# Kernel tuning notes

Hardware: AMD Instinct MI355X
Metric: run time of the kernel (lower is better)

The kernel has to match this reference:

```python
import jax, jax.numpy as jnp
import numpy as np

N_EMBD = 384
NUM_HEADS = 6


def setup_inputs() -> dict:
    key = jax.random.key(0)
    k1, k2, k3 = jax.random.split(key, 3)
    b, t = 128, 256
    X = jax.random.normal(k1, (b, t, N_EMBD), dtype=jnp.float32)
    Wqkv = jax.random.normal(k2, (N_EMBD, 3 * N_EMBD), dtype=jnp.float32) * 0.02
    Wproj = jax.random.normal(k3, (N_EMBD, N_EMBD), dtype=jnp.float32) * 0.02
    return {"X": X, "Wqkv": Wqkv, "Wproj": Wproj}


def reference(X, Wqkv, Wproj):
    b, t, c = X.shape
    d = c // NUM_HEADS
    # fused QKV projection; split order in the source is K, Q, V
    qkv = X @ Wqkv  # (b, t, 3c)
    K, Q, V = jnp.split(qkv, 3, axis=-1)
    # (b, t, H, d) -> (b, H, t, d)
    K = K.reshape(b, t, NUM_HEADS, d).transpose(0, 2, 1, 3)
    Q = Q.reshape(b, t, NUM_HEADS, d).transpose(0, 2, 1, 3)
    V = V.reshape(b, t, NUM_HEADS, d).transpose(0, 2, 1, 3)
    # NOTE: faithful quirk — scale by full embed dim c, not head_size
    scale = c ** (-0.5)
    W = jnp.einsum("bhqd,bhkd->bhqk", Q, K) * scale  # (b, H, t, t)
    causal = jnp.tril(jnp.ones((t, t), dtype=bool))
    W = jnp.where(causal, W, -jnp.inf)
    W = jax.nn.softmax(W, axis=-1)
    # dropout layers are identity in eval mode
    OUT = jnp.einsum("bhqk,bhkd->bhqd", W, V)  # (b, H, t, d)
    OUT = OUT.transpose(0, 2, 1, 3).reshape(b, t, c)
    return OUT @ Wproj
```

## Files before the change

### kernel.cpp

```cpp
#include <hip/hip_runtime.h>
#include <hip/hip_bf16.h>

#define BATCH 128
#define TSEQ  256
#define NEMBD 384
#define NHEAD 6
#define HDIM  64
#define C3    1152
#define MROWS 32768
#define KGTOT 48
#define NBH   768
#define BHSZ  16384

#define NA_CH  (MROWS * KGTOT)
#define NW1_CH (C3 * KGTOT)
#define NW2_CH (NEMBD * KGTOT)

#define XBLOCKS 2048
#define WBLOCKS 288

typedef __attribute__((ext_vector_type(8))) short short8v;
typedef __attribute__((ext_vector_type(4))) float float4v;


__device__ __forceinline__ float bf2f(unsigned short u) {
  union { unsigned int i; float f; } x;
  x.i = ((unsigned int)u) << 16;
  return x.f;
}

__device__ __forceinline__ unsigned short f2bf(float f) {
  __hip_bfloat16 h = __float2bfloat16(f);
  unsigned short u;
  __builtin_memcpy(&u, &h, 2);
  return u;
}

__device__ __forceinline__ void convB_body(const float* __restrict__ W,
                                           unsigned short* __restrict__ out,
                                           int N, int idx) {
  const int nl  = idx & 127;
  const int kgg = (idx >> 7) % KGTOT;
  const int nb  = idx / (128 * KGTOT);
  const int n = nb * 128 + nl;
  short8v v;
#pragma unroll
  for (int j = 0; j < 8; ++j)
    v[j] = (short)f2bf(W[(size_t)(kgg * 8 + j) * N + n]);
  *reinterpret_cast<short8v*>(out + (size_t)idx * 8) = v;
}

__global__ __launch_bounds__(256)
void convert_all(const float* __restrict__ X, const float* __restrict__ W1,
                 const float* __restrict__ W2, unsigned short* __restrict__ Abf,
                 unsigned short* __restrict__ W1T, unsigned short* __restrict__ W2T) {
  const int tid = threadIdx.x;
  if (blockIdx.x < XBLOCKS) {
    __shared__ __attribute__((aligned(16))) unsigned short T[16][392];
    const int rb = blockIdx.x;
    const float* Xb = X + (size_t)rb * 16 * NEMBD;
#pragma unroll
    for (int i = 0; i < 6; ++i) {
      const int f4 = i * 256 + tid;
      const float4 v = reinterpret_cast<const float4*>(Xb)[f4];
      const int r = f4 / 96;
      const int c = (f4 % 96) * 4;
      ushort4 u;
      u.x = f2bf(v.x); u.y = f2bf(v.y); u.z = f2bf(v.z); u.w = f2bf(v.w);
      *reinterpret_cast<ushort4*>(&T[r][c]) = u;
    }
    __syncthreads();
#pragma unroll
    for (int i = 0; i < 3; ++i) {
      const int c2   = i * 256 + tid;
      const int kgg  = c2 >> 4;
      const int ml16 = c2 & 15;
      const short8v v = *reinterpret_cast<const short8v*>(&T[ml16][kgg * 8]);
      const int m  = rb * 16 + ml16;
      const int mb = m >> 7;
      const int ml = m & 127;
      *reinterpret_cast<short8v*>(Abf + ((size_t)(mb * KGTOT + kgg) * 128 + ml) * 8) = v;
    }
  } else {
    const int wi = (blockIdx.x - XBLOCKS) * 256 + tid;
    if (wi < NW1_CH) convB_body(W1, W1T, C3, wi);
    else             convB_body(W2, W2T, NEMBD, wi - NW1_CH);
  }
}


#define GEMM_STAGE(Ab, Bb, kb, ASL, BSL)                                               \
  _Pragma("unroll") for (int r = 0; r < 2; ++r) {                                      \
    const int i = r * 256 + tid;                                                       \
    const size_t goff = ((size_t)((kb) * 4 + (i >> 7)) * 128 + (i & 127)) * 8;         \
    __builtin_amdgcn_global_load_lds(                                                  \
        (const __attribute__((address_space(1))) unsigned int*)((Ab) + goff),          \
        (__attribute__((address_space(3))) unsigned int*)((ASL) + i * 8), 16, 0, 0);   \
    __builtin_amdgcn_global_load_lds(                                                  \
        (const __attribute__((address_space(1))) unsigned int*)((Bb) + goff),          \
        (__attribute__((address_space(3))) unsigned int*)((BSL) + i * 8), 16, 0, 0);   \
  }

#define GEMM_CORE(Ab, Bb)                                                              \
  __shared__ __attribute__((aligned(16))) unsigned short S[16384];                     \
  const int tid  = threadIdx.x;                                                        \
  const int wave = tid >> 6;                                                           \
  const int lane = tid & 63;                                                           \
  const int wm  = (wave & 1) * 64;                                                     \
  const int wn  = (wave >> 1) * 64;                                                    \
  const int l15 = lane & 15;                                                           \
  const int lq  = lane >> 4;                                                           \
  float4v acc[4][4];                                                                   \
  _Pragma("unroll") for (int i = 0; i < 4; ++i)                                        \
    _Pragma("unroll") for (int j = 0; j < 4; ++j)                                      \
      acc[i][j] = (float4v){0.f, 0.f, 0.f, 0.f};                                       \
  GEMM_STAGE(Ab, Bb, 0, S, S + 4096)                                                   \
  for (int kb = 0; kb < KGTOT / 4; ++kb) {                                             \
    const int cur = (kb & 1) * 8192;                                                   \
    const int nxt = 8192 - cur;                                                        \
    __syncthreads();                                                                   \
    if (kb + 1 < KGTOT / 4) {                                                          \
      GEMM_STAGE(Ab, Bb, kb + 1, S + nxt, S + nxt + 4096)                              \
    }                                                                                  \
    short8v af[4], bfr[4];                                                             \
    _Pragma("unroll") for (int mi = 0; mi < 4; ++mi)                                   \
      af[mi] = *reinterpret_cast<const short8v*>(                                      \
          S + cur + (size_t)(lq * 128 + wm + mi * 16 + l15) * 8);                      \
    _Pragma("unroll") for (int ni = 0; ni < 4; ++ni)                                   \
      bfr[ni] = *reinterpret_cast<const short8v*>(                                     \
          S + cur + 4096 + (size_t)(lq * 128 + wn + ni * 16 + l15) * 8);               \
    _Pragma("unroll") for (int mi = 0; mi < 4; ++mi)                                   \
      _Pragma("unroll") for (int ni = 0; ni < 4; ++ni)                                 \
        acc[mi][ni] = __builtin_amdgcn_mfma_f32_16x16x32_bf16(af[mi], bfr[ni],         \
                                                              acc[mi][ni], 0, 0, 0);   \
  }

__global__ __launch_bounds__(256)
void gemm_qkv(const unsigned short* __restrict__ A,
              const unsigned short* __restrict__ B,
              unsigned short* __restrict__ KQV) {
  const int ord   = blockIdx.x;
  const int xcd   = ord & 7;
  const int g     = ord >> 3;
  const int mtile = xcd * 32 + (g & 31);
  const int ntile = g >> 5;
  const unsigned short* Ab = A + (size_t)mtile * (KGTOT * 128 * 8);
  const unsigned short* Bb = B + (size_t)ntile * (KGTOT * 128 * 8);
  GEMM_CORE(Ab, Bb)
  const int colb = ntile * 128 + wn + l15;
  const int rowb = mtile * 128 + wm + lq * 4;
  if (ntile >= 6) {
    unsigned short* Vb = KQV + (size_t)(2 * NBH) * BHSZ;
#pragma unroll
    for (int ni = 0; ni < 4; ++ni) {
      const int rem = colb + ni * 16 - 768;
      const int hh  = rem >> 6;
      const int d   = rem & 63;
#pragma unroll
      for (int mi = 0; mi < 4; ++mi) {
        const int m  = rowb + mi * 16;
        const int bb = m >> 8;
        const int tt = m & 255;
        ushort4 v;
        v.x = f2bf(acc[mi][ni][0]); v.y = f2bf(acc[mi][ni][1]);
        v.z = f2bf(acc[mi][ni][2]); v.w = f2bf(acc[mi][ni][3]);
        *reinterpret_cast<ushort4*>(
            Vb + (size_t)(bb * NHEAD + hh) * BHSZ + (tt >> 3) * 512 + d * 8 + (tt & 7)) = v;
      }
    }
  } else {
    const int type = (ntile >= 3) ? 1 : 0;
    const float sc = type ? 0.051031036307982884f : 1.0f;
    unsigned short* outb = KQV + (size_t)type * NBH * BHSZ;
    const int hp = ntile - type * 3;
    const int bb = mtile >> 1;
    const int t0 = (mtile & 1) * 128;
    __syncthreads();
#pragma unroll
    for (int ni = 0; ni < 4; ++ni) {
      const int lc = wn + ni * 16 + l15;
      const int c8 = lc >> 3;
      const int dl = lc & 7;
#pragma unroll
      for (int mi = 0; mi < 4; ++mi) {
        const int lr0 = wm + lq * 4 + mi * 16;
#pragma unroll
        for (int r = 0; r < 4; ++r)
          S[(size_t)(c8 * 128 + lr0 + r) * 8 + dl] = f2bf(acc[mi][ni][r] * sc);
      }
    }
    __syncthreads();
#pragma unroll
    for (int it = 0; it < 8; ++it) {
      const int f  = it * 2048 + tid * 8;
      const int c8 = f >> 10;
      const int lr = (f >> 3) & 127;
      const int hh = hp * 2 + (c8 >> 3);
      const int dg = c8 & 7;
      *reinterpret_cast<short8v*>(
          outb + (size_t)(bb * NHEAD + hh) * BHSZ + dg * 2048 + (size_t)(t0 + lr) * 8) =
          *reinterpret_cast<const short8v*>(S + f);
    }
  }
}

__global__ __launch_bounds__(256)
void gemm_proj(const unsigned short* __restrict__ A,
               const unsigned short* __restrict__ B,
               float* __restrict__ C, int N) {
  const int ord   = blockIdx.x;
  const int xcd   = ord & 7;
  const int g     = ord >> 3;
  const int mtile = xcd * 32 + (g & 31);
  const int ntile = g >> 5;
  const unsigned short* Ab = A + (size_t)mtile * (KGTOT * 128 * 8);
  const unsigned short* Bb = B + (size_t)ntile * (KGTOT * 128 * 8);
  GEMM_CORE(Ab, Bb)
  float* Sf = reinterpret_cast<float*>(S);
#pragma unroll
  for (int pass = 0; pass < 2; ++pass) {
    __syncthreads();
    if ((wave & 1) == pass) {
#pragma unroll
      for (int mi = 0; mi < 4; ++mi)
#pragma unroll
        for (int ni = 0; ni < 4; ++ni)
#pragma unroll
          for (int r = 0; r < 4; ++r)
            Sf[(lq * 4 + mi * 16 + r) * 128 + (wn + ni * 16 + l15)] = acc[mi][ni][r];
    }
    __syncthreads();
    const int rowstart = mtile * 128 + pass * 64;
#pragma unroll
    for (int it = 0; it < 8; ++it) {
      const int f  = it * 1024 + tid * 4;
      const int lr = f >> 7;
      const int lc = f & 127;
      *reinterpret_cast<float4*>(&C[(size_t)(rowstart + lr) * N + ntile * 128 + lc]) =
          *reinterpret_cast<const float4*>(&Sf[f]);
    }
  }
}

__global__ __launch_bounds__(256, 3)
void attn_mfma(const unsigned short* __restrict__ KQV,
               unsigned short* __restrict__ Obf) {
  const int bh   = blockIdx.x;
  const int b    = bh / NHEAD;
  const int h    = bh - b * NHEAD;
  const int tid  = threadIdx.x;
  const int wave = tid >> 6;
  const int lane = tid & 63;
  const int l15  = lane & 15;
  const int lq   = lane >> 4;

  __shared__ __attribute__((aligned(16))) unsigned short Kls[16384];
  __shared__ __attribute__((aligned(16))) unsigned short Pt[4][1024];

  const unsigned short* Kb = KQV + (size_t)bh * BHSZ;
  const unsigned short* Qb = KQV + (size_t)(NBH + bh) * BHSZ;
  const unsigned short* Vb = KQV + (size_t)(2 * NBH + bh) * BHSZ;

#pragma unroll
  for (int r = 0; r < 8; ++r) {
    const int i = r * 256 + tid;
    __builtin_amdgcn_global_load_lds(
        (const __attribute__((address_space(1))) unsigned int*)(Kb + (size_t)i * 8),
        (__attribute__((address_space(3))) unsigned int*)(Kls + i * 8), 16, 0, 0);
  }
  __syncthreads();

  unsigned short* Pw = Pt[wave];

  for (int j = 0; j < 4; ++j) {
    short8v qa[2];
#pragma unroll
    for (int s = 0; s < 2; ++s)
      qa[s] = *reinterpret_cast<const short8v*>(
          Qb + (size_t)(s * 4 + lq) * 2048 + (size_t)(j * 64 + wave * 16 + l15) * 8);

    float4v o[4];
#pragma unroll
    for (int nf = 0; nf < 4; ++nf) o[nf] = (float4v){0.f, 0.f, 0.f, 0.f};
    float4v lp = (float4v){0.f, 0.f, 0.f, 0.f};

    for (int kt = 0; kt <= j; ++kt) {
      short8v vf[2][4];
#pragma unroll
      for (int s = 0; s < 2; ++s)
#pragma unroll
        for (int nf = 0; nf < 4; ++nf)
          vf[s][nf] = *reinterpret_cast<const short8v*>(
              Vb + (size_t)(kt * 8 + s * 4 + lq) * 512 + (size_t)(nf * 16 + l15) * 8);

      float4v sf[4];
#pragma unroll
      for (int nf = 0; nf < 4; ++nf) sf[nf] = (float4v){0.f, 0.f, 0.f, 0.f};
#pragma unroll
      for (int s = 0; s < 2; ++s) {
        short8v kf[4];
#pragma unroll
        for (int nf = 0; nf < 4; ++nf)
          kf[nf] = *reinterpret_cast<const short8v*>(
              Kls + (size_t)(s * 4 + lq) * 2048 + (size_t)(kt * 64 + nf * 16 + l15) * 8);
#pragma unroll
        for (int nf = 0; nf < 4; ++nf)
          sf[nf] = __builtin_amdgcn_mfma_f32_16x16x32_bf16(qa[s], kf[nf], sf[nf], 0, 0, 0);
      }

      if (kt == j) {
        const int qit = wave * 16 + lq * 4;
#pragma unroll
        for (int nf = 0; nf < 4; ++nf) {
          const int key = nf * 16 + l15;
#pragma unroll
          for (int r = 0; r < 4; ++r)
            if (key > qit + r) sf[nf][r] = -INFINITY;
        }
      }

#pragma unroll
      for (int nf = 0; nf < 4; ++nf) {
        const int kg  = nf * 2 + (l15 >> 3);
        const int pos = l15 & 7;
#pragma unroll
        for (int r = 0; r < 4; ++r) {
          const float p = __expf(sf[nf][r]);
          lp[r] += p;
          Pw[(kg * 16 + lq * 4 + r) * 8 + pos] = f2bf(p);
        }
      }

#pragma unroll
      for (int s = 0; s < 2; ++s) {
        short8v pa = *reinterpret_cast<const short8v*>(
            Pw + (size_t)((s * 4 + lq) * 16 + l15) * 8);
#pragma unroll
        for (int nf = 0; nf < 4; ++nf)
          o[nf] = __builtin_amdgcn_mfma_f32_16x16x32_bf16(pa, vf[s][nf], o[nf], 0, 0, 0);
      }
    }

#pragma unroll
    for (int off = 1; off <= 8; off <<= 1)
#pragma unroll
      for (int r = 0; r < 4; ++r)
        lp[r] += __shfl_xor(lp[r], off);
    float4v inv;
#pragma unroll
    for (int r = 0; r < 4; ++r) inv[r] = 1.f / lp[r];

    const int tq = j * 64 + wave * 16 + lq * 4;
#pragma unroll
    for (int nf = 0; nf < 4; ++nf) {
      const int d   = nf * 16 + l15;
      const int gg  = h * 8 + (d >> 3);
      const int pos = d & 7;
#pragma unroll
      for (int r = 0; r < 4; ++r) {
        const int m = b * TSEQ + tq + r;
        Obf[((size_t)(m >> 7) * KGTOT + gg) * 1024 + (size_t)(m & 127) * 8 + pos] =
            f2bf(o[nf][r] * inv[r]);
      }
    }
  }
}


extern "C" void kernel_launch(void* const* d_in, const int* in_sizes, int n_in,
                              void* d_out, int out_size, void* d_ws, size_t ws_size,
                              hipStream_t stream) {
  const float* X     = (const float*)d_in[0];
  const float* Wqkv  = (const float*)d_in[1];
  const float* Wproj = (const float*)d_in[2];
  float* out = (float*)d_out;

  unsigned short* KQV    = (unsigned short*)d_ws;
  unsigned short* Abf    = (unsigned short*)((char*)d_ws + 75497472);
  unsigned short* WqkvT  = (unsigned short*)((char*)d_ws + 75497472 + 25165824);
  unsigned short* WprojT = (unsigned short*)((char*)d_ws + 75497472 + 25165824 + 884736);
  unsigned short* Obf    = Abf;

  dim3 blk(256);
  convert_all<<<dim3(XBLOCKS + WBLOCKS), blk, 0, stream>>>(
      X, Wqkv, Wproj, Abf, WqkvT, WprojT);
  gemm_qkv<<<dim3(2304), blk, 0, stream>>>(Abf, WqkvT, KQV);
  attn_mfma<<<dim3(NBH), blk, 0, stream>>>(KQV, Obf);
  gemm_proj<<<dim3(768), blk, 0, stream>>>(Obf, WprojT, out, NEMBD);
}
```

Baseline: 180.2 us.

## Fuse X fp32-to-bf16 conversion into QKV GEMM A-tile staging

Removes the separate pass that converted X to a blocked bf16 layout. The QKV GEMM now loads fp32 X directly into registers, converts it and writes the bf16 tile into LDS, software-pipelined one k-block ahead. This drops a full write and re-read of the 25 MB bf16 copy of X and shrinks the first kernel to weights only. In exchange, each of the 9 n-tiles re-reads the fp32 A rows, doubling the bytes per A load, and adds register pressure plus conversion work inside the GEMM loop.

```diff
diff --git a/kernel.cpp b/kernel.cpp
--- a/kernel.cpp
+++ b/kernel.cpp
@@ -12,22 +12,13 @@
 #define NBH   768
 #define BHSZ  16384
 
-#define NA_CH  (MROWS * KGTOT)
 #define NW1_CH (C3 * KGTOT)
 #define NW2_CH (NEMBD * KGTOT)
-
-#define XBLOCKS 2048
 #define WBLOCKS 288
 
 typedef __attribute__((ext_vector_type(8))) short short8v;
 typedef __attribute__((ext_vector_type(4))) float float4v;
 
-
-__device__ __forceinline__ float bf2f(unsigned short u) {
-  union { unsigned int i; float f; } x;
-  x.i = ((unsigned int)u) << 16;
-  return x.f;
-}
 
 __device__ __forceinline__ unsigned short f2bf(float f) {
   __hip_bfloat16 h = __float2bfloat16(f);
@@ -51,41 +42,11 @@
 }
 
 __global__ __launch_bounds__(256)
-void convert_all(const float* __restrict__ X, const float* __restrict__ W1,
-                 const float* __restrict__ W2, unsigned short* __restrict__ Abf,
-                 unsigned short* __restrict__ W1T, unsigned short* __restrict__ W2T) {
-  const int tid = threadIdx.x;
-  if (blockIdx.x < XBLOCKS) {
-    __shared__ __attribute__((aligned(16))) unsigned short T[16][392];
-    const int rb = blockIdx.x;
-    const float* Xb = X + (size_t)rb * 16 * NEMBD;
-#pragma unroll
-    for (int i = 0; i < 6; ++i) {
-      const int f4 = i * 256 + tid;
-      const float4 v = reinterpret_cast<const float4*>(Xb)[f4];
-      const int r = f4 / 96;
-      const int c = (f4 % 96) * 4;
-      ushort4 u;
-      u.x = f2bf(v.x); u.y = f2bf(v.y); u.z = f2bf(v.z); u.w = f2bf(v.w);
-      *reinterpret_cast<ushort4*>(&T[r][c]) = u;
-    }
-    __syncthreads();
-#pragma unroll
-    for (int i = 0; i < 3; ++i) {
-      const int c2   = i * 256 + tid;
-      const int kgg  = c2 >> 4;
-      const int ml16 = c2 & 15;
-      const short8v v = *reinterpret_cast<const short8v*>(&T[ml16][kgg * 8]);
-      const int m  = rb * 16 + ml16;
-      const int mb = m >> 7;
-      const int ml = m & 127;
-      *reinterpret_cast<short8v*>(Abf + ((size_t)(mb * KGTOT + kgg) * 128 + ml) * 8) = v;
-    }
-  } else {
-    const int wi = (blockIdx.x - XBLOCKS) * 256 + tid;
-    if (wi < NW1_CH) convB_body(W1, W1T, C3, wi);
-    else             convB_body(W2, W2T, NEMBD, wi - NW1_CH);
-  }
+void convert_w(const float* __restrict__ W1, const float* __restrict__ W2,
+               unsigned short* __restrict__ W1T, unsigned short* __restrict__ W2T) {
+  const int wi = blockIdx.x * 256 + threadIdx.x;
+  if (wi < NW1_CH) convB_body(W1, W1T, C3, wi);
+  else             convB_body(W2, W2T, NEMBD, wi - NW1_CH);
 }
 
 
@@ -135,8 +96,36 @@
                                                               acc[mi][ni], 0, 0, 0);   \
   }
 
+
+#define STAGE_A_LOAD(kb, xv)                                                           \
+  _Pragma("unroll") for (int p = 0; p < 4; ++p) {                                      \
+    const int f4 = p * 256 + tid;                                                      \
+    xv[p] = *reinterpret_cast<const float4*>(                                          \
+        Xb + (size_t)(f4 >> 3) * NEMBD + (kb) * 32 + (f4 & 7) * 4);                    \
+  }
+
+#define STAGE_A_WRITE(xv, ASL)                                                         \
+  _Pragma("unroll") for (int p = 0; p < 4; ++p) {                                      \
+    const int f4  = p * 256 + tid;                                                     \
+    const int row = f4 >> 3;                                                           \
+    const int c4  = f4 & 7;                                                            \
+    ushort4 u;                                                                         \
+    u.x = f2bf(xv[p].x); u.y = f2bf(xv[p].y);                                          \
+    u.z = f2bf(xv[p].z); u.w = f2bf(xv[p].w);                                          \
+    *reinterpret_cast<ushort4*>((ASL) + ((c4 >> 1) * 128 + row) * 8 + (c4 & 1) * 4) = u; \
+  }
+
+#define STAGE_B(Bb, kb, BSL)                                                           \
+  _Pragma("unroll") for (int r = 0; r < 2; ++r) {                                      \
+    const int i = r * 256 + tid;                                                       \
+    const size_t goff = ((size_t)((kb) * 4 + (i >> 7)) * 128 + (i & 127)) * 8;         \
+    __builtin_amdgcn_global_load_lds(                                                  \
+        (const __attribute__((address_space(1))) unsigned int*)((Bb) + goff),          \
+        (__attribute__((address_space(3))) unsigned int*)((BSL) + i * 8), 16, 0, 0);   \
+  }
+
 __global__ __launch_bounds__(256)
-void gemm_qkv(const unsigned short* __restrict__ A,
+void gemm_qkv(const float* __restrict__ X,
               const unsigned short* __restrict__ B,
               unsigned short* __restrict__ KQV) {
   const int ord   = blockIdx.x;
@@ -144,9 +133,59 @@
   const int g     = ord >> 3;
   const int mtile = xcd * 32 + (g & 31);
   const int ntile = g >> 5;
-  const unsigned short* Ab = A + (size_t)mtile * (KGTOT * 128 * 8);
+  const float* Xb = X + (size_t)mtile * 128 * NEMBD;
   const unsigned short* Bb = B + (size_t)ntile * (KGTOT * 128 * 8);
-  GEMM_CORE(Ab, Bb)
+
+  __shared__ __attribute__((aligned(16))) unsigned short S[16384];
+  const int tid  = threadIdx.x;
+  const int wave = tid >> 6;
+  const int lane = tid & 63;
+  const int wm  = (wave & 1) * 64;
+  const int wn  = (wave >> 1) * 64;
+  const int l15 = lane & 15;
+  const int lq  = lane >> 4;
+  float4v acc[4][4];
+#pragma unroll
+  for (int i = 0; i < 4; ++i)
+#pragma unroll
+    for (int j = 0; j < 4; ++j)
+      acc[i][j] = (float4v){0.f, 0.f, 0.f, 0.f};
+
+  {
+    float4 xv0[4];
+    STAGE_A_LOAD(0, xv0)
+    STAGE_B(Bb, 0, S + 4096)
+    STAGE_A_WRITE(xv0, S)
+  }
+  for (int kb = 0; kb < KGTOT / 4; ++kb) {
+    const int cur = (kb & 1) * 8192;
+    const int nxt = 8192 - cur;
+    __syncthreads();
+    float4 xv[4];
+    if (kb + 1 < KGTOT / 4) {
+      STAGE_A_LOAD(kb + 1, xv)
+      STAGE_B(Bb, kb + 1, S + nxt + 4096)
+    }
+    short8v af[4], bfr[4];
+#pragma unroll
+    for (int mi = 0; mi < 4; ++mi)
+      af[mi] = *reinterpret_cast<const short8v*>(
+          S + cur + (size_t)(lq * 128 + wm + mi * 16 + l15) * 8);
+#pragma unroll
+    for (int ni = 0; ni < 4; ++ni)
+      bfr[ni] = *reinterpret_cast<const short8v*>(
+          S + cur + 4096 + (size_t)(lq * 128 + wn + ni * 16 + l15) * 8);
+#pragma unroll
+    for (int mi = 0; mi < 4; ++mi)
+#pragma unroll
+      for (int ni = 0; ni < 4; ++ni)
+        acc[mi][ni] = __builtin_amdgcn_mfma_f32_16x16x32_bf16(af[mi], bfr[ni],
+                                                              acc[mi][ni], 0, 0, 0);
+    if (kb + 1 < KGTOT / 4) {
+      STAGE_A_WRITE(xv, S + nxt)
+    }
+  }
+
   const int colb = ntile * 128 + wn + l15;
   const int rowb = mtile * 128 + wm + lq * 4;
   if (ntile >= 6) {
@@ -376,15 +415,13 @@
   float* out = (float*)d_out;
 
   unsigned short* KQV    = (unsigned short*)d_ws;
-  unsigned short* Abf    = (unsigned short*)((char*)d_ws + 75497472);
+  unsigned short* Obf    = (unsigned short*)((char*)d_ws + 75497472);
   unsigned short* WqkvT  = (unsigned short*)((char*)d_ws + 75497472 + 25165824);
   unsigned short* WprojT = (unsigned short*)((char*)d_ws + 75497472 + 25165824 + 884736);
-  unsigned short* Obf    = Abf;
 
   dim3 blk(256);
-  convert_all<<<dim3(XBLOCKS + WBLOCKS), blk, 0, stream>>>(
-      X, Wqkv, Wproj, Abf, WqkvT, WprojT);
-  gemm_qkv<<<dim3(2304), blk, 0, stream>>>(Abf, WqkvT, KQV);
+  convert_w<<<dim3(WBLOCKS), blk, 0, stream>>>(Wqkv, Wproj, WqkvT, WprojT);
+  gemm_qkv<<<dim3(2304), blk, 0, stream>>>(X, WqkvT, KQV);
   attn_mfma<<<dim3(NBH), blk, 0, stream>>>(KQV, Obf);
   gemm_proj<<<dim3(768), blk, 0, stream>>>(Obf, WprojT, out, NEMBD);
 }
```

Result: slower. 188.8 us (+4.8%).

## Stage V and attention output stores through LDS with swizzled layouts

Applied to the files above, without the earlier changes.

The V part of the QKV GEMM epilogue now goes through shared memory and is written out as coalesced 16-byte stores, where before each lane did scattered 8-byte stores. The K/Q staging buffer gets an XOR swizzle to reduce LDS bank conflicts. The attention kernel now stages its per-wave output tile in its P buffer with a swizzle and writes 16-byte vectors instead of scalar 2-byte stores. This adds barriers and LDS traffic, and the swizzle indexing has to line up exactly between writes and reads.

```diff
diff --git a/kernel.cpp b/kernel.cpp
--- a/kernel.cpp
+++ b/kernel.cpp
@@ -22,12 +22,6 @@
 typedef __attribute__((ext_vector_type(8))) short short8v;
 typedef __attribute__((ext_vector_type(4))) float float4v;
 
-
-__device__ __forceinline__ float bf2f(unsigned short u) {
-  union { unsigned int i; float f; } x;
-  x.i = ((unsigned int)u) << 16;
-  return x.f;
-}
 
 __device__ __forceinline__ unsigned short f2bf(float f) {
   __hip_bfloat16 h = __float2bfloat16(f);
@@ -147,26 +141,40 @@
   const unsigned short* Ab = A + (size_t)mtile * (KGTOT * 128 * 8);
   const unsigned short* Bb = B + (size_t)ntile * (KGTOT * 128 * 8);
   GEMM_CORE(Ab, Bb)
-  const int colb = ntile * 128 + wn + l15;
-  const int rowb = mtile * 128 + wm + lq * 4;
   if (ntile >= 6) {
     unsigned short* Vb = KQV + (size_t)(2 * NBH) * BHSZ;
+    const int hh0 = (ntile - 6) * 2;
+    const int bb  = mtile >> 1;
+    const int tg0 = (mtile & 1) * 16;
+    __syncthreads();
 #pragma unroll
     for (int ni = 0; ni < 4; ++ni) {
-      const int rem = colb + ni * 16 - 768;
-      const int hh  = rem >> 6;
-      const int d   = rem & 63;
+      const int lc = wn + ni * 16 + l15;
+      const int hh = lc >> 6;
+      const int d  = lc & 63;
 #pragma unroll
       for (int mi = 0; mi < 4; ++mi) {
-        const int m  = rowb + mi * 16;
-        const int bb = m >> 8;
-        const int tt = m & 255;
-        ushort4 v;
-        v.x = f2bf(acc[mi][ni][0]); v.y = f2bf(acc[mi][ni][1]);
-        v.z = f2bf(acc[mi][ni][2]); v.w = f2bf(acc[mi][ni][3]);
+        const int ttl = wm + mi * 16 + lq * 4;
+        const int tg  = ttl >> 3;
+        const int tl0 = ttl & 7;
+        ushort4 u;
+        u.x = f2bf(acc[mi][ni][0]); u.y = f2bf(acc[mi][ni][1]);
+        u.z = f2bf(acc[mi][ni][2]); u.w = f2bf(acc[mi][ni][3]);
         *reinterpret_cast<ushort4*>(
-            Vb + (size_t)(bb * NHEAD + hh) * BHSZ + (tt >> 3) * 512 + d * 8 + (tt & 7)) = v;
-      }
+            S + (size_t)(((hh * 16 + tg) * 64 + d) * 8 + tl0)) = u;
+      }
+    }
+    __syncthreads();
+#pragma unroll
+    for (int it = 0; it < 8; ++it) {
+      const int f  = it * 2048 + tid * 8;
+      const int cc = f >> 3;
+      const int d  = cc & 63;
+      const int tg = (cc >> 6) & 15;
+      const int hh = cc >> 10;
+      *reinterpret_cast<short8v*>(
+          Vb + (size_t)(bb * NHEAD + hh0 + hh) * BHSZ + (tg0 + tg) * 512 + d * 8) =
+          *reinterpret_cast<const short8v*>(S + f);
     }
   } else {
     const int type = (ntile >= 3) ? 1 : 0;
@@ -185,21 +193,26 @@
       for (int mi = 0; mi < 4; ++mi) {
         const int lr0 = wm + lq * 4 + mi * 16;
 #pragma unroll
-        for (int r = 0; r < 4; ++r)
-          S[(size_t)(c8 * 128 + lr0 + r) * 8 + dl] = f2bf(acc[mi][ni][r] * sc);
+        for (int r = 0; r < 4; ++r) {
+          const int c  = c8 * 128 + lr0 + r;
+          const int cs = c ^ (((c >> 7) ^ (c >> 3)) & 7);
+          S[(size_t)cs * 8 + dl] = f2bf(acc[mi][ni][r] * sc);
+        }
       }
     }
     __syncthreads();
 #pragma unroll
     for (int it = 0; it < 8; ++it) {
-      const int f  = it * 2048 + tid * 8;
-      const int c8 = f >> 10;
-      const int lr = (f >> 3) & 127;
-      const int hh = hp * 2 + (c8 >> 3);
-      const int dg = c8 & 7;
+      const int f   = it * 2048 + tid * 8;
+      const int cc  = f >> 3;
+      const int cs  = cc ^ (((cc >> 7) ^ (cc >> 3)) & 7);
+      const int c8  = cc >> 7;
+      const int lr  = cc & 127;
+      const int hh  = hp * 2 + (c8 >> 3);
+      const int dg  = c8 & 7;
       *reinterpret_cast<short8v*>(
           outb + (size_t)(bb * NHEAD + hh) * BHSZ + dg * 2048 + (size_t)(t0 + lr) * 8) =
-          *reinterpret_cast<const short8v*>(S + f);
+          *reinterpret_cast<const short8v*>(S + (size_t)cs * 8);
     }
   }
 }
@@ -350,18 +363,27 @@
 #pragma unroll
     for (int r = 0; r < 4; ++r) inv[r] = 1.f / lp[r];
 
-    const int tq = j * 64 + wave * 16 + lq * 4;
 #pragma unroll
     for (int nf = 0; nf < 4; ++nf) {
       const int d   = nf * 16 + l15;
-      const int gg  = h * 8 + (d >> 3);
+      const int ggl = d >> 3;
       const int pos = d & 7;
 #pragma unroll
       for (int r = 0; r < 4; ++r) {
-        const int m = b * TSEQ + tq + r;
-        Obf[((size_t)(m >> 7) * KGTOT + gg) * 1024 + (size_t)(m & 127) * 8 + pos] =
-            f2bf(o[nf][r] * inv[r]);
-      }
+        const int chunk = (ggl * 16 + lq * 4 + r) ^ ggl;
+        Pw[chunk * 8 + pos] = f2bf(o[nf][r] * inv[r]);
+      }
+    }
+    const int mb  = b * 2 + (j >> 1);
+    const int ml0 = (j & 1) * 64 + wave * 16;
+#pragma unroll
+    for (int t = 0; t < 2; ++t) {
+      const int cc  = t * 64 + lane;
+      const int ggl = cc >> 4;
+      const int mll = cc & 15;
+      *reinterpret_cast<short8v*>(
+          Obf + ((size_t)(mb * KGTOT) + h * 8 + ggl) * 1024 + (size_t)(ml0 + mll) * 8) =
+          *reinterpret_cast<const short8v*>(Pw + (size_t)(cc ^ ggl) * 8);
     }
   }
 }
```

Measured after the change: 173.6 us. 3.7% less time.
